# Kernel optimization log

Hardware: AMD Instinct MI355X
Metric: run time of the kernel (lower is better)

The kernel has to match this reference:

```python
import jax, jax.numpy as jnp
import numpy as np

N_NODES = 50000
N_EDGES = 800000
F = 53
B = 128
H = 4


def _p(key, shape, scale=0.1):
    return jax.random.normal(key, shape, dtype=jnp.float32) * scale


def setup_inputs() -> dict:
    key = jax.random.key(0)
    ks = jax.random.split(key, 40)
    inp = {
        'x': jax.random.normal(ks[0], (N_NODES, F), dtype=jnp.float32),
        'edge_index': jax.random.randint(ks[1], (2, N_EDGES), 0, N_NODES),
        'batch': jnp.sort(jax.random.randint(ks[2], (N_NODES,), 0, B)),
        # GATConv(53 -> 53, heads=4)
        'gat_w': _p(ks[3], (F, H * F)),
        'gat_att_src': _p(ks[4], (H, F)),
        'gat_att_dst': _p(ks[5], (H, F)),
        'gat_bias': _p(ks[6], (H * F,)),
        # GINConv MLP: 53 -> 106 -> 106
        'gin_w1': _p(ks[7], (F, 2 * F)), 'gin_b1': _p(ks[8], (2 * F,)),
        'gin_w2': _p(ks[9], (2 * F, 2 * F)), 'gin_b2': _p(ks[10], (2 * F,)),
        # EdgeConv MLP: 106 -> 106 -> 106
        'ec_w1': _p(ks[11], (2 * F, 2 * F)), 'ec_b1': _p(ks[12], (2 * F,)),
        'ec_w2': _p(ks[13], (2 * F, 2 * F)), 'ec_b2': _p(ks[14], (2 * F,)),
        # per-branch heads
        'fg1_w': _p(ks[15], (4 * F, 256)), 'fg1_b': _p(ks[16], (256,)),
        'fg2_w': _p(ks[17], (256, 128)), 'fg2_b': _p(ks[18], (128,)),
        'fg3_w': _p(ks[19], (2 * F, 256)), 'fg3_b': _p(ks[20], (256,)),
        'fg4_w': _p(ks[21], (256, 128)), 'fg4_b': _p(ks[22], (128,)),
        'fg5_w': _p(ks[23], (2 * F, 256)), 'fg5_b': _p(ks[24], (256,)),
        'fg6_w': _p(ks[25], (256, 128)), 'fg6_b': _p(ks[26], (128,)),
        # final MLP
        'fc1_w': _p(ks[27], (384, 128)), 'fc1_b': _p(ks[28], (128,)),
        'fc2_w': _p(ks[29], (128, 64)), 'fc2_b': _p(ks[30], (64,)),
        'out_w': _p(ks[31], (64, 1)), 'out_b': _p(ks[32], (1,)),
    }
    return inp


def _gat(x, src, dst, w, a_src, a_dst, bias):
    # PyG GATConv with add_self_loops=True, negative_slope=0.2, concat heads
    n = x.shape[0]
    loop = jnp.arange(n)
    s = jnp.concatenate([src, loop])
    d = jnp.concatenate([dst, loop])
    xh = (x @ w).reshape(n, H, F)                      # [N,H,F]
    al_s = jnp.einsum('nhf,hf->nh', xh, a_src)         # [N,H]
    al_d = jnp.einsum('nhf,hf->nh', xh, a_dst)
    e = jax.nn.leaky_relu(al_s[s] + al_d[d], 0.2)      # [E2,H]
    m = jax.ops.segment_max(e, d, num_segments=n)
    ex = jnp.exp(e - m[d])
    z = jax.ops.segment_sum(ex, d, num_segments=n)
    alpha = ex / (z[d] + 1e-16)                        # softmax over in-edges
    msg = xh[s] * alpha[:, :, None]                    # [E2,H,F]
    out = jax.ops.segment_sum(msg, d, num_segments=n)
    return out.reshape(n, H * F) + bias


def _gin(x, src, dst, w1, b1, w2, b2):
    # PyG GINConv, eps=0: nn(x + sum_j x_j)
    n = x.shape[0]
    agg = jax.ops.segment_sum(x[src], dst, num_segments=n)
    h = x + agg
    return jax.nn.relu(h @ w1 + b1) @ w2 + b2


def _edgeconv(x, src, dst, w1, b1, w2, b2):
    # PyG EdgeConv: max_j nn([x_i, x_j - x_i]) at target i
    n = x.shape[0]
    xi = x[dst]
    feat = jnp.concatenate([xi, x[src] - xi], axis=-1)  # [E,2F]
    h = jax.nn.relu(feat @ w1 + b1) @ w2 + b2
    out = jax.ops.segment_max(h, dst, num_segments=n)
    return jnp.where(jnp.isfinite(out), out, 0.0)       # empty segments -> 0


def _gep(x, batch):
    # global mean pool per graph
    s = jax.ops.segment_sum(x, batch, num_segments=B)
    cnt = jax.ops.segment_sum(jnp.ones((x.shape[0],), x.dtype), batch, num_segments=B)
    return s / jnp.maximum(cnt, 1.0)[:, None]


def reference(x, edge_index, batch,
              gat_w, gat_att_src, gat_att_dst, gat_bias,
              gin_w1, gin_b1, gin_w2, gin_b2,
              ec_w1, ec_b1, ec_w2, ec_b2,
              fg1_w, fg1_b, fg2_w, fg2_b, fg3_w, fg3_b,
              fg4_w, fg4_b, fg5_w, fg5_b, fg6_w, fg6_b,
              fc1_w, fc1_b, fc2_w, fc2_b, out_w, out_b):
    relu = jax.nn.relu
    src, dst = edge_index[0], edge_index[1]

    xt = relu(_gat(x, src, dst, gat_w, gat_att_src, gat_att_dst, gat_bias))
    xt = _gep(xt, batch)
    xt = relu(xt @ fg1_w + fg1_b)
    xt = relu(xt @ fg2_w + fg2_b)

    xt2 = relu(_gin(x, src, dst, gin_w1, gin_b1, gin_w2, gin_b2))
    xt2 = _gep(xt2, batch)
    xt2 = relu(xt2 @ fg3_w + fg3_b)
    xt2 = relu(xt2 @ fg4_w + fg4_b)

    xt3 = relu(_edgeconv(x, src, dst, ec_w1, ec_b1, ec_w2, ec_b2))
    xt3 = _gep(xt3, batch)
    xt3 = relu(xt3 @ fg5_w + fg5_b)
    xt3 = relu(xt3 @ fg6_w + fg6_b)

    h = jnp.concatenate([xt, xt2, xt3], axis=1)         # [B,384]
    h = relu(h @ fc1_w + fc1_b)
    h = relu(h @ fc2_w + fc2_b)
    return jax.nn.sigmoid(h @ out_w + out_b)            # [B,1]
```

## Files before the change

kernel.cpp:

```cpp
#include <hip/hip_runtime.h>
#include <hip/hip_bf16.h>
#include <math.h>

#define N_NODES 50000
#define N_EDGES 800000
#define FDIM 53
#define BATCH 128
#define HF 212
#define F2 106
#define POOLW 424
#define NPK2 220
#define PSTR 32
#define ECS 128

typedef __attribute__((ext_vector_type(8))) short short8;
typedef __attribute__((ext_vector_type(4))) float f32x4;

__device__ __forceinline__ float leaky02(float x){ return x >= 0.f ? x : 0.2f * x; }

__device__ __forceinline__ short f2bf(float x) {
  unsigned u = __float_as_uint(x);
  unsigned r = (u + 0x7fffu + ((u >> 16) & 1u)) >> 16;
  return (short)r;
}
__device__ __forceinline__ float bf2f(short b) {
  return __uint_as_float(((unsigned)(unsigned short)b) << 16);
}
__device__ __forceinline__ unsigned pk2(float a, float b) {
  union { __hip_bfloat162 h; unsigned u; } c;
  c.h = __float22bfloat162_rn(make_float2(a, b));
  return c.u;
}
__device__ __forceinline__ void ldsbar() {
  __builtin_amdgcn_s_waitcnt(0xC07F);
  __builtin_amdgcn_s_barrier();
}

__global__ void k_prep(const float* __restrict__ ec_w1, const float* __restrict__ ec_b1,
                       const float* __restrict__ gat_w, const float* __restrict__ asrc,
                       const float* __restrict__ adst,
                       float* __restrict__ Wp, float* __restrict__ bp) {
  int idx = blockIdx.x * blockDim.x + threadIdx.x;
  if (idx < FDIM * NPK2) {
    int k = idx / NPK2, j = idx % NPK2;
    float v;
    if (j < F2)            v = ec_w1[k * F2 + j] - ec_w1[(FDIM + k) * F2 + j];
    else if (j < 2 * F2)   v = ec_w1[(FDIM + k) * F2 + (j - F2)];
    else {
      int r = j - 2 * F2;
      int sd = r >> 2, h = r & 3;
      const float* av = sd ? adst : asrc;
      float acc = 0.f;
      for (int f = 0; f < FDIM; ++f)
        acc += gat_w[k * HF + h * FDIM + f] * av[h * FDIM + f];
      v = acc;
    }
    Wp[idx] = v;
  }
  if (idx < NPK2) {
    bp[idx] = (idx < F2) ? ec_b1[idx] : 0.f;
  }
}

#define GM 64
#define GN 110
#define GNP 112
#define APAD 57
__global__ __launch_bounds__(256) void k_gemm(
    const float* __restrict__ x, const float* __restrict__ Wp, const float* __restrict__ bp,
    short* __restrict__ xb, short* __restrict__ Ub, short* __restrict__ Vb,
    float* __restrict__ alS, float* __restrict__ alD) {
  __shared__ float As[GM * APAD];
  __shared__ float Ws[FDIM * GNP];
  int mb = blockIdx.x >> 1, nc = blockIdx.x & 1;
  int m0 = mb * GM, n0 = nc * GN;
  int t = threadIdx.x;
  for (int idx = t; idx < GM * FDIM; idx += 256) {
    int m = idx / FDIM, k = idx % FDIM;
    int gm = m0 + m;
    float v = (gm < N_NODES) ? x[(size_t)gm * FDIM + k] : 0.f;
    As[m * APAD + k] = v;
    if (nc == 0 && gm < N_NODES) xb[(size_t)gm * 64 + k] = f2bf(v);
  }
  for (int idx = t; idx < FDIM * GNP; idx += 256) {
    int k = idx / GNP, n = idx % GNP;
    Ws[idx] = (n < GN) ? Wp[k * NPK2 + n0 + n] : 0.f;
  }
  __syncthreads();
  int tx = t & 15, ty = t >> 4;
  int ms = tx * 4, ns = ty * 7;
  float acc[4][7];
#pragma unroll
  for (int i = 0; i < 4; i++)
#pragma unroll
    for (int j = 0; j < 7; j++) acc[i][j] = 0.f;
  for (int k = 0; k < FDIM; k++) {
    float a0 = As[(ms + 0) * APAD + k];
    float a1 = As[(ms + 1) * APAD + k];
    float a2 = As[(ms + 2) * APAD + k];
    float a3 = As[(ms + 3) * APAD + k];
    float b[7];
#pragma unroll
    for (int j = 0; j < 7; j++) b[j] = Ws[k * GNP + ns + j];
#pragma unroll
    for (int j = 0; j < 7; j++) {
      acc[0][j] += a0 * b[j];
      acc[1][j] += a1 * b[j];
      acc[2][j] += a2 * b[j];
      acc[3][j] += a3 * b[j];
    }
  }
  float bj[7];
#pragma unroll
  for (int j = 0; j < 7; j++) {
    int g = n0 + ns + j;
    bj[j] = (g < NPK2) ? bp[g] : 0.f;
  }
#pragma unroll
  for (int i = 0; i < 4; i++) {
    int gm = m0 + ms + i;
    if (gm >= N_NODES) break;
#pragma unroll
    for (int j = 0; j < 7; j++) {
      int g = n0 + ns + j;
      float v = acc[i][j] + bj[j];
      if (g < F2)             Ub[(size_t)gm * ECS + g] = f2bf(v);
      else if (g < 2 * F2)    Vb[(size_t)gm * ECS + (g - F2)] = f2bf(v);
      else if (g < 2 * F2 + 4) alS[gm * 4 + (g - 2 * F2)] = v;
      else if (g < NPK2)      alD[gm * 4 + (g - 2 * F2 - 4)] = v;
    }
  }
}

#define SCAN_BLOCKS ((N_NODES + 255) / 256)

__global__ void k_hist(const int* __restrict__ ei, int* __restrict__ histP) {
  int t = blockIdx.x * blockDim.x + threadIdx.x;
  if (t < N_EDGES) atomicAdd(&histP[ei[N_EDGES + t] << 5], 1);
}

__global__ __launch_bounds__(256) void k_scan1(const int* __restrict__ histP,
                                               const int* __restrict__ batch,
                                               int* __restrict__ rp, int* __restrict__ bsum,
                                               int* __restrict__ start) {
  __shared__ int buf[256];
  int tid = threadIdx.x;
  int idx = blockIdx.x * 256 + tid;
  int v = (idx < N_NODES) ? histP[idx << 5] : 0;
  buf[tid] = v;
  __syncthreads();
  for (int off = 1; off < 256; off <<= 1) {
    int t2 = (tid >= off) ? buf[tid - off] : 0;
    __syncthreads();
    buf[tid] += t2;
    __syncthreads();
  }
  if (idx < N_NODES) rp[idx] = buf[tid] - v;
  if (tid == 255) bsum[blockIdx.x] = buf[255];
  if (idx < N_NODES) {
    int b = batch[idx];
    if (idx == 0)
      for (int g = 0; g <= b; g++) start[g] = 0;
    int bn = (idx + 1 < N_NODES) ? batch[idx + 1] : BATCH;
    for (int g = b + 1; g <= bn; g++) start[g] = idx + 1;
  }
}

__global__ __launch_bounds__(256) void k_scan3(const int* __restrict__ bsum,
                                               int* __restrict__ rp, int* __restrict__ histP) {
  __shared__ int buf[256];
  int tid = threadIdx.x;
  int v = (tid < SCAN_BLOCKS) ? bsum[tid] : 0;
  buf[tid] = v;
  __syncthreads();
  for (int off = 1; off < 256; off <<= 1) {
    int t2 = (tid >= off) ? buf[tid - off] : 0;
    __syncthreads();
    buf[tid] += t2;
    __syncthreads();
  }
  int boff = (blockIdx.x == 0) ? 0 : buf[blockIdx.x - 1];
  int idx = blockIdx.x * 256 + tid;
  if (idx < N_NODES) {
    int o = rp[idx] + boff;
    rp[idx] = o;
    histP[idx << 5] = o;
  }
  if (idx == 0) rp[N_NODES] = N_EDGES;
}

__global__ void k_scatter(const int* __restrict__ ei, int* __restrict__ histP,
                          int* __restrict__ colidx) {
  int e = blockIdx.x * blockDim.x + threadIdx.x;
  if (e >= N_EDGES) return;
  int d = ei[N_EDGES + e];
  int pos = atomicAdd(&histP[d << 5], 1);
  colidx[pos] = ei[e];
}

#define GCH 20
__global__ __launch_bounds__(256) void k_gatgin(
    const short* __restrict__ xb, const float* __restrict__ alS, const float* __restrict__ alD,
    const int* __restrict__ rp, const int* __restrict__ colidx,
    short* __restrict__ agg4, float* __restrict__ agg) {
  int wid = threadIdx.x >> 6, lane = threadIdx.x & 63;
  bool fa = lane < FDIM;
  int i0 = blockIdx.x * GCH;
  int iend = min(i0 + GCH, N_NODES);
  __shared__ int rpG[GCH + 1];
  __shared__ int sL[4][64];
  __shared__ float4 eL[4][64];
  {
    int t = threadIdx.x, nn = iend - i0;
    if (t <= nn) rpG[t] = rp[i0 + t];
  }
  __syncthreads();
  for (int i = i0 + wid; i < iend; i += 4) {
    int base = rpG[i - i0], deg = rpG[i - i0 + 1] - base;
    float4 adv = *(const float4*)(alD + (size_t)i * 4);
    float4 asv = *(const float4*)(alS + (size_t)i * 4);
    float aldi[4] = {adv.x, adv.y, adv.z, adv.w};
    float exs[4];
    exs[0] = __expf(leaky02(asv.x + aldi[0]));
    exs[1] = __expf(leaky02(asv.y + aldi[1]));
    exs[2] = __expf(leaky02(asv.z + aldi[2]));
    exs[3] = __expf(leaky02(asv.w + aldi[3]));
    float xiv = fa ? bf2f(xb[(size_t)i * 64 + lane]) : 0.f;
    float ag0 = exs[0] * xiv, ag1 = exs[1] * xiv, ag2 = exs[2] * xiv, ag3 = exs[3] * xiv;
    float ax = xiv;
    float zl[4] = {0.f, 0.f, 0.f, 0.f};

    for (int c0 = 0; c0 < deg; c0 += 64) {
      int cn = min(64, deg - c0);
      int s = 0;
      float ex0 = 0.f, ex1 = 0.f, ex2 = 0.f, ex3 = 0.f;
      if (lane < cn) {
        s = colidx[base + c0 + lane];
        float4 av = *(const float4*)(alS + (size_t)s * 4);
        ex0 = __expf(leaky02(av.x + aldi[0]));
        ex1 = __expf(leaky02(av.y + aldi[1]));
        ex2 = __expf(leaky02(av.z + aldi[2]));
        ex3 = __expf(leaky02(av.w + aldi[3]));
        zl[0] += ex0; zl[1] += ex1; zl[2] += ex2; zl[3] += ex3;
      }
      sL[wid][lane] = s;
      eL[wid][lane] = make_float4(ex0, ex1, ex2, ex3);
      for (int jj = 0; jj < cn; jj += 4) {
        int4 s4 = *(const int4*)&sL[wid][jj];
        int sj[4] = {s4.x, s4.y, s4.z, s4.w};
        float4 e0 = eL[wid][jj + 0];
        float4 e1 = eL[wid][jj + 1];
        float4 e2 = eL[wid][jj + 2];
        float4 e3 = eL[wid][jj + 3];
        float xg[4];
#pragma unroll
        for (int q = 0; q < 4; q++)
          xg[q] = fa ? bf2f(xb[(size_t)sj[q] * 64 + lane]) : 0.f;
        ag0 += e0.x * xg[0] + e1.x * xg[1] + e2.x * xg[2] + e3.x * xg[3];
        ag1 += e0.y * xg[0] + e1.y * xg[1] + e2.y * xg[2] + e3.y * xg[3];
        ag2 += e0.z * xg[0] + e1.z * xg[1] + e2.z * xg[2] + e3.z * xg[3];
        ag3 += e0.w * xg[0] + e1.w * xg[1] + e2.w * xg[2] + e3.w * xg[3];
#pragma unroll
        for (int q = 0; q < 4; q++)
          if (jj + q < cn) ax += xg[q];
      }
    }
#pragma unroll
    for (int off = 32; off >= 1; off >>= 1)
#pragma unroll
      for (int h = 0; h < 4; h++) zl[h] += __shfl_xor(zl[h], off);
    if (fa) {
      float z0 = zl[0] + exs[0] + 1e-16f;
      float z1 = zl[1] + exs[1] + 1e-16f;
      float z2 = zl[2] + exs[2] + 1e-16f;
      float z3 = zl[3] + exs[3] + 1e-16f;
      short* ar = agg4 + (size_t)i * HF;
      ar[0 * FDIM + lane] = f2bf(ag0 / z0);
      ar[1 * FDIM + lane] = f2bf(ag1 / z1);
      ar[2 * FDIM + lane] = f2bf(ag2 / z2);
      ar[3 * FDIM + lane] = f2bf(ag3 / z3);
      agg[(size_t)i * FDIM + lane] = ax;
    }
  }
}

#define AHS 264
#define BTS 72
#define A2PAD 111
#define SMBYTES 75904
__global__ __launch_bounds__(256) void k_post(
    const short* __restrict__ agg4, const float* __restrict__ gat_w,
    const float* __restrict__ gat_b,
    const float* __restrict__ agg,
    const float* __restrict__ w1, const float* __restrict__ b1,
    const float* __restrict__ w2, const float* __restrict__ b2,
    const int* __restrict__ batch, float* __restrict__ pooled) {
  __shared__ __align__(16) char smraw[SMBYTES];
  __shared__ float psum[4 * 224];
  __shared__ int batL[64];
  int m0 = blockIdx.x * 64;
  int t = threadIdx.x;
  const int lane = t & 63, wid = t >> 6;
  const int n16 = lane & 15, quad = lane >> 4;

  {
    short* Ah = (short*)smraw;
    short* Bt = (short*)(smraw + (size_t)64 * AHS * 2);
    for (int idx = t; idx < 4 * 224; idx += 256) psum[idx] = 0.f;
    if (t < 64) batL[t] = (m0 + t < N_NODES) ? batch[m0 + t] : 0;
    for (int idx = t; idx < 64 * 256; idx += 256) {
      int node = idx >> 8, rem = idx & 255;
      int h = rem >> 6, k = rem & 63;
      int gm = m0 + node;
      short v = (k < FDIM && gm < N_NODES) ? agg4[(size_t)gm * HF + h * FDIM + k] : (short)0;
      Ah[node * AHS + h * 64 + k] = v;
    }
    for (int idx = t; idx < 4 * 56 * 64; idx += 256) {
      int h = idx / (56 * 64), rem = idx % (56 * 64);
      int n = rem >> 6, k = rem & 63;
      short v = (k < FDIM && n < FDIM) ? f2bf(gat_w[k * HF + h * FDIM + n]) : (short)0;
      Bt[(h * 56 + n) * BTS + k] = v;
    }
    __syncthreads();
    const int mrow0 = wid * 16;
    const int bmin = batL[0];
#pragma unroll
    for (int h = 0; h < 4; h++) {
      short8 af0 = *(const short8*)&Ah[(mrow0 + n16) * AHS + h * 64 + quad * 8];
      short8 af1 = *(const short8*)&Ah[(mrow0 + n16) * AHS + h * 64 + 32 + quad * 8];
#pragma unroll
      for (int nt = 0; nt < 4; nt++) {
        short8 b0 = *(const short8*)&Bt[(h * 56 + nt * 16 + n16) * BTS + quad * 8];
        short8 b1 = *(const short8*)&Bt[(h * 56 + nt * 16 + n16) * BTS + 32 + quad * 8];
        f32x4 acc = {0.f, 0.f, 0.f, 0.f};
        acc = __builtin_amdgcn_mfma_f32_16x16x32_bf16(af0, b0, acc, 0, 0, 0);
        acc = __builtin_amdgcn_mfma_f32_16x16x32_bf16(af1, b1, acc, 0, 0, 0);
        int jn = nt * 16 + n16;
        bool jv = jn < FDIM;
        float bj = jv ? gat_b[h * FDIM + jn] : 0.f;
        float pj = 0.f; int curb = -1;
#pragma unroll
        for (int r = 0; r < 4; r++) {
          int lm = mrow0 + quad * 4 + r;
          int gm = m0 + lm;
          if (gm < N_NODES) {
            float o = fmaxf(acc[r] + bj, 0.f);
            int b = batL[lm];
            if (b != curb) {
              if (curb >= 0 && jv) {
                int slot = curb - bmin;
                if (slot >= 0 && slot < 4) atomicAdd(&psum[slot * 224 + h * 56 + jn], pj);
                else atomicAdd(&pooled[(size_t)curb * POOLW + h * FDIM + jn], pj);
              }
              curb = b; pj = o;
            } else {
              pj += o;
            }
          }
        }
        if (curb >= 0 && jv) {
          int slot = curb - bmin;
          if (slot >= 0 && slot < 4) atomicAdd(&psum[slot * 224 + h * 56 + jn], pj);
          else atomicAdd(&pooled[(size_t)curb * POOLW + h * FDIM + jn], pj);
        }
      }
    }
    __syncthreads();
    for (int idx = t; idx < 4 * 224; idx += 256) {
      int slot = idx / 224, c = idx % 224;
      int h = c / 56, jn = c % 56;
      float v = psum[idx];
      int b = bmin + slot;
      if (jn < FDIM && b < BATCH && v != 0.f)
        atomicAdd(&pooled[(size_t)b * POOLW + h * FDIM + jn], v);
    }
    __syncthreads();
  }

  {
    float* B1 = (float*)smraw;
    float* Hs = (float*)(smraw + (size_t)F2 * 112 * 4);
    float* As = B1;
    float* Ws1 = B1 + 64 * APAD;
    for (int idx = t; idx < 4 * 112; idx += 256) psum[idx] = 0.f;
    for (int idx = t; idx < 64 * FDIM; idx += 256) {
      int m = idx / FDIM, k = idx % FDIM;
      int gm = m0 + m;
      As[m * APAD + k] = (gm < N_NODES) ? agg[(size_t)gm * FDIM + k] : 0.f;
    }
    for (int idx = t; idx < FDIM * 112; idx += 256) {
      int k = idx / 112, n = idx % 112;
      Ws1[idx] = (n < F2) ? w1[k * F2 + n] : 0.f;
    }
    __syncthreads();
    int tx = t & 15, ty = t >> 4;
    int ms = tx * 4, ns = ty * 7;
    {
      float acc[4][7];
#pragma unroll
      for (int i = 0; i < 4; i++)
#pragma unroll
        for (int j = 0; j < 7; j++) acc[i][j] = 0.f;
      for (int k = 0; k < FDIM; k++) {
        float a0 = As[(ms + 0) * APAD + k];
        float a1 = As[(ms + 1) * APAD + k];
        float a2 = As[(ms + 2) * APAD + k];
        float a3 = As[(ms + 3) * APAD + k];
        float b[7];
#pragma unroll
        for (int j = 0; j < 7; j++) b[j] = Ws1[k * 112 + ns + j];
#pragma unroll
        for (int j = 0; j < 7; j++) {
          acc[0][j] += a0 * b[j];
          acc[1][j] += a1 * b[j];
          acc[2][j] += a2 * b[j];
          acc[3][j] += a3 * b[j];
        }
      }
#pragma unroll
      for (int i = 0; i < 4; i++) {
#pragma unroll
        for (int j = 0; j < 7; j++) {
          int n = ns + j;
          if (n < F2) Hs[(ms + i) * A2PAD + n] = fmaxf(acc[i][j] + b1[n], 0.f);
        }
      }
    }
    __syncthreads();
    for (int idx = t; idx < F2 * 112; idx += 256) {
      int k = idx / 112, n = idx % 112;
      B1[idx] = (n < F2) ? w2[k * F2 + n] : 0.f;
    }
    __syncthreads();
    float acc[4][7];
#pragma unroll
    for (int i = 0; i < 4; i++)
#pragma unroll
      for (int j = 0; j < 7; j++) acc[i][j] = 0.f;
    for (int k = 0; k < F2; k++) {
      float a0 = Hs[(ms + 0) * A2PAD + k];
      float a1 = Hs[(ms + 1) * A2PAD + k];
      float a2 = Hs[(ms + 2) * A2PAD + k];
      float a3 = Hs[(ms + 3) * A2PAD + k];
      float b[7];
#pragma unroll
      for (int j = 0; j < 7; j++) b[j] = B1[k * 112 + ns + j];
#pragma unroll
      for (int j = 0; j < 7; j++) {
        acc[0][j] += a0 * b[j];
        acc[1][j] += a1 * b[j];
        acc[2][j] += a2 * b[j];
        acc[3][j] += a3 * b[j];
      }
    }
    float b2n[7];
#pragma unroll
    for (int j = 0; j < 7; j++) {
      int n = ns + j;
      b2n[j] = (n < F2) ? b2[n] : 0.f;
    }
    int bmin = batL[0];
    float pj[7];
#pragma unroll
    for (int j = 0; j < 7; j++) pj[j] = 0.f;
    int curb = -1;
#pragma unroll
    for (int i = 0; i < 4; i++) {
      int gm = m0 + ms + i;
      if (gm >= N_NODES) break;
      int b = batL[ms + i];
      if (b != curb) {
        if (curb >= 0) {
          int slot = curb - bmin;
          if (slot >= 0 && slot < 4) {
#pragma unroll
            for (int j = 0; j < 7; j++)
              if (ns + j < F2) atomicAdd(&psum[slot * 112 + ns + j], pj[j]);
          } else {
            float* pg = pooled + (size_t)curb * POOLW + HF;
#pragma unroll
            for (int j = 0; j < 7; j++)
              if (ns + j < F2) atomicAdd(&pg[ns + j], pj[j]);
          }
        }
        curb = b;
#pragma unroll
        for (int j = 0; j < 7; j++)
          pj[j] = (ns + j < F2) ? fmaxf(acc[i][j] + b2n[j], 0.f) : 0.f;
      } else {
#pragma unroll
        for (int j = 0; j < 7; j++)
          if (ns + j < F2) pj[j] += fmaxf(acc[i][j] + b2n[j], 0.f);
      }
    }
    if (curb >= 0) {
      int slot = curb - bmin;
      if (slot >= 0 && slot < 4) {
#pragma unroll
        for (int j = 0; j < 7; j++)
          if (ns + j < F2) atomicAdd(&psum[slot * 112 + ns + j], pj[j]);
      } else {
        float* pg = pooled + (size_t)curb * POOLW + HF;
#pragma unroll
        for (int j = 0; j < 7; j++)
          if (ns + j < F2) atomicAdd(&pg[ns + j], pj[j]);
      }
    }
    __syncthreads();
    for (int idx = t; idx < 4 * 112; idx += 256) {
      int slot = idx / 112, n = idx % 112;
      float v = psum[idx];
      int b = bmin + slot;
      if (n < F2 && b < BATCH && v != 0.f)
        atomicAdd(&pooled[(size_t)b * POOLW + HF + n], v);
    }
  }
}

#define ECH 25
__global__ __launch_bounds__(256) void k_ec(
    const short* __restrict__ Ub, const short* __restrict__ Vb,
    const float* __restrict__ w2, const float* __restrict__ b2,
    const int* __restrict__ rp, const int* __restrict__ colidx,
    const int* __restrict__ batch, float* __restrict__ pooled) {
  const int t = threadIdx.x;
  const int lane = t & 63, wid = t >> 6;
  const int n16 = lane & 15, quad = lane >> 4;
  const int nt = (wid == 3) ? 1 : 2;

  const int i0 = blockIdx.x * ECH;
  const int iend = min(i0 + ECH, N_NODES);
  const int nn = iend - i0;

  __shared__ int rpL[ECH + 1];
  __shared__ int batL[ECH];

  short8 Bh[2][4];
  for (int tt = 0; tt < 2; tt++) {
    int ucol = (wid * 2 + tt) * 16 + n16;
    for (int kc = 0; kc < 4; kc++) {
      short8 vh;
#pragma unroll
      for (int jv = 0; jv < 8; jv++) {
        int kk = kc * 32 + quad * 8 + jv;
        float w = (ucol < F2 && kk < F2) ? w2[kk * F2 + ucol] : 0.f;
        vh[jv] = f2bf(w);
      }
      Bh[tt][kc] = vh;
    }
  }
  float b2v[2];
#pragma unroll
  for (int tt = 0; tt < 2; tt++) {
    int u = (wid * 2 + tt) * 16 + n16;
    b2v[tt] = (u < F2) ? b2[u] : 0.f;
  }

  if (t <= nn) rpL[t] = rp[i0 + t];
  if (t < nn) batL[t] = batch[i0 + t];
  __syncthreads();

  __shared__ short hs[2][16 * 16 * 8];
  union SU { short8 s; unsigned u[4]; };
  const int es = t & 15, kg = t >> 4;
  const int k0 = kg * 8;

  float sm0 = 0.f, sm1 = 0.f;
  int curb = -1;
  const int u0 = (wid * 2) * 16 + n16;
  const int u1 = (wid * 2 + 1) * 16 + n16;

  auto advance = [&](int& ii, int& ttb, int& bb, int& dd) -> bool {
    ttb++;
    if (ttb * 16 < dd) return true;
    ttb = 0;
    for (ii = ii + 1; ii < iend; ii++) {
      bb = rpL[ii - i0]; dd = rpL[ii - i0 + 1] - bb;
      if (dd > 0) return true;
    }
    return false;
  };

  int i = i0, tb = 0, base = 0, deg = 0;
  bool have = false;
  for (; i < iend; i++) {
    base = rpL[i - i0]; deg = rpL[i - i0 + 1] - base;
    if (deg > 0) { have = true; break; }
  }
  short8 pu8{}, pv8{};
  int i1 = i, tb1 = 0, base1 = base, deg1 = deg;
  bool have1 = false;
  int sc = 0;
  if (have) {
    pu8 = *(const short8*)(Ub + (size_t)i * ECS + k0);
    int s0 = colidx[base + ((es < deg) ? es : 0)];
    pv8 = *(const short8*)(Vb + (size_t)s0 * ECS + k0);
    have1 = advance(i1, tb1, base1, deg1);
    if (have1) {
      int eg = tb1 * 16 + es;
      sc = colidx[base1 + ((eg < deg1) ? eg : 0)];
    }
  }

  float Uc[8];
  float vmax0 = -1e30f, vmax1 = -1e30f;
  int parity = 0;
  while (have) {
    if (tb == 0) {
#pragma unroll
      for (int j = 0; j < 8; j++) Uc[j] = bf2f(pu8[j]);
    }
    SU w;
#pragma unroll
    for (int p = 0; p < 4; p++) {
      bool kv = (k0 + 2 * p) < F2;
      float h0 = kv ? fmaxf(Uc[2 * p]     + bf2f(pv8[2 * p]),     0.f) : 0.f;
      float h1 = kv ? fmaxf(Uc[2 * p + 1] + bf2f(pv8[2 * p + 1]), 0.f) : 0.f;
      w.u[p] = pk2(h0, h1);
    }
    *(short8*)&hs[parity][(kg * 16 + es) * 8] = w.s;

    int i2 = i1, tb2 = tb1, base2 = base1, deg2 = deg1;
    bool have2 = false;
    int scN = 0;
    if (have1) {
      if (tb1 == 0) pu8 = *(const short8*)(Ub + (size_t)i1 * ECS + k0);
      pv8 = *(const short8*)(Vb + (size_t)sc * ECS + k0);
      have2 = advance(i2, tb2, base2, deg2);
      if (have2) {
        int eg2 = tb2 * 16 + es;
        scN = colidx[base2 + ((eg2 < deg2) ? eg2 : 0)];
      }
    }

    ldsbar();
    f32x4 a0 = {0.f, 0.f, 0.f, 0.f}, a1 = {0.f, 0.f, 0.f, 0.f};
#pragma unroll
    for (int kc = 0; kc < 4; kc++) {
      short8 af = *(const short8*)&hs[parity][((kc * 4 + quad) * 16 + n16) * 8];
      a0 = __builtin_amdgcn_mfma_f32_16x16x32_bf16(af, Bh[0][kc], a0, 0, 0, 0);
      if (nt > 1)
        a1 = __builtin_amdgcn_mfma_f32_16x16x32_bf16(af, Bh[1][kc], a1, 0, 0, 0);
    }
#pragma unroll
    for (int r = 0; r < 4; r++) {
      int er = tb * 16 + quad * 4 + r;
      if (er < deg) { vmax0 = fmaxf(vmax0, a0[r]); vmax1 = fmaxf(vmax1, a1[r]); }
    }
    if (!have1 || i1 != i) {
      vmax0 = fmaxf(vmax0, __shfl_xor(vmax0, 16));
      vmax0 = fmaxf(vmax0, __shfl_xor(vmax0, 32));
      vmax1 = fmaxf(vmax1, __shfl_xor(vmax1, 16));
      vmax1 = fmaxf(vmax1, __shfl_xor(vmax1, 32));
      float o0 = fmaxf(vmax0 + b2v[0], 0.f);
      float o1 = fmaxf(vmax1 + b2v[1], 0.f);
      int b = batL[i - i0];
      if (b != curb) {
        if (curb >= 0 && quad == 0) {
          float* pg = pooled + (size_t)curb * POOLW + HF + F2;
          if (u0 < F2) atomicAdd(&pg[u0], sm0);
          if (nt > 1 && u1 < F2) atomicAdd(&pg[u1], sm1);
        }
        curb = b; sm0 = o0; sm1 = o1;
      } else {
        sm0 += o0; sm1 += o1;
      }
      vmax0 = -1e30f; vmax1 = -1e30f;
    }
    i = i1; tb = tb1; base = base1; deg = deg1; have = have1;
    i1 = i2; tb1 = tb2; base1 = base2; deg1 = deg2; have1 = have2;
    sc = scN;
    parity ^= 1;
  }
  if (curb >= 0 && quad == 0) {
    float* pg = pooled + (size_t)curb * POOLW + HF + F2;
    if (u0 < F2) atomicAdd(&pg[u0], sm0);
    if (nt > 1 && u1 < F2) atomicAdd(&pg[u1], sm1);
  }
}

__global__ __launch_bounds__(256) void k_heads(
    const float* __restrict__ pooled, const int* __restrict__ start,
    const float* __restrict__ fg1_w, const float* __restrict__ fg1_b,
    const float* __restrict__ fg2_w, const float* __restrict__ fg2_b,
    const float* __restrict__ fg3_w, const float* __restrict__ fg3_b,
    const float* __restrict__ fg4_w, const float* __restrict__ fg4_b,
    const float* __restrict__ fg5_w, const float* __restrict__ fg5_b,
    const float* __restrict__ fg6_w, const float* __restrict__ fg6_b,
    const float* __restrict__ fc1_w, const float* __restrict__ fc1_b,
    const float* __restrict__ fc2_w, const float* __restrict__ fc2_b,
    const float* __restrict__ out_w, const float* __restrict__ out_b,
    float* __restrict__ out) {
  int g = blockIdx.x, t = threadIdx.x;
  __shared__ float in[POOLW];
  __shared__ float mid[256];
  __shared__ float cat[384];
  __shared__ float h1[128];
  __shared__ float h2[64];
  float c = fmaxf((float)(start[g + 1] - start[g]), 1.f);
  for (int idx = t; idx < POOLW; idx += 256)
    in[idx] = pooled[(size_t)g * POOLW + idx] / c;
  __syncthreads();
  const float* w1s[3] = {fg1_w, fg3_w, fg5_w};
  const float* b1s[3] = {fg1_b, fg3_b, fg5_b};
  const float* w2s[3] = {fg2_w, fg4_w, fg6_w};
  const float* b2s[3] = {fg2_b, fg4_b, fg6_b};
  const int off[4] = {0, HF, HF + F2, POOLW};
  for (int br = 0; br < 3; br++) {
    int kin = off[br + 1] - off[br];
    const float* iv = &in[off[br]];
    float a = b1s[br][t];
    const float* W = w1s[br];
    for (int k = 0; k < kin; k++) a += iv[k] * W[k * 256 + t];
    mid[t] = fmaxf(a, 0.f);
    __syncthreads();
    if (t < 128) {
      float b = b2s[br][t];
      const float* W2 = w2s[br];
      for (int k = 0; k < 256; k++) b += mid[k] * W2[k * 128 + t];
      cat[br * 128 + t] = fmaxf(b, 0.f);
    }
    __syncthreads();
  }
  if (t < 128) {
    float a = fc1_b[t];
    for (int k = 0; k < 384; k++) a += cat[k] * fc1_w[k * 128 + t];
    h1[t] = fmaxf(a, 0.f);
  }
  __syncthreads();
  if (t < 64) {
    float a = fc2_b[t];
    for (int k = 0; k < 128; k++) a += h1[k] * fc2_w[k * 64 + t];
    h2[t] = fmaxf(a, 0.f);
  }
  __syncthreads();
  if (t == 0) {
    float a = out_b[0];
    for (int k = 0; k < 64; k++) a += h2[k] * out_w[k];
    out[g] = 1.f / (1.f + __expf(-a));
  }
}

extern "C" void kernel_launch(void* const* d_in, const int* in_sizes, int n_in,
                              void* d_out, int out_size, void* d_ws, size_t ws_size,
                              hipStream_t stream) {
  const float* x      = (const float*)d_in[0];
  const int*   ei     = (const int*)d_in[1];
  const int*   batch  = (const int*)d_in[2];
  const float* gat_w  = (const float*)d_in[3];
  const float* asrc   = (const float*)d_in[4];
  const float* adst   = (const float*)d_in[5];
  const float* gat_b  = (const float*)d_in[6];
  const float* gin_w1 = (const float*)d_in[7];
  const float* gin_b1 = (const float*)d_in[8];
  const float* gin_w2 = (const float*)d_in[9];
  const float* gin_b2 = (const float*)d_in[10];
  const float* ec_w1  = (const float*)d_in[11];
  const float* ec_b1  = (const float*)d_in[12];
  const float* ec_w2  = (const float*)d_in[13];
  const float* ec_b2  = (const float*)d_in[14];
  const float* fg1_w = (const float*)d_in[15]; const float* fg1_b = (const float*)d_in[16];
  const float* fg2_w = (const float*)d_in[17]; const float* fg2_b = (const float*)d_in[18];
  const float* fg3_w = (const float*)d_in[19]; const float* fg3_b = (const float*)d_in[20];
  const float* fg4_w = (const float*)d_in[21]; const float* fg4_b = (const float*)d_in[22];
  const float* fg5_w = (const float*)d_in[23]; const float* fg5_b = (const float*)d_in[24];
  const float* fg6_w = (const float*)d_in[25]; const float* fg6_b = (const float*)d_in[26];
  const float* fc1_w = (const float*)d_in[27]; const float* fc1_b = (const float*)d_in[28];
  const float* fc2_w = (const float*)d_in[29]; const float* fc2_b = (const float*)d_in[30];
  const float* out_w = (const float*)d_in[31]; const float* out_b = (const float*)d_in[32];
  float* out = (float*)d_out;

  char* ws = (char*)d_ws;
  size_t off = 0;
  auto alloc = [&](size_t bytes) -> void* {
    void* p = ws + off;
    off = (off + bytes + 255) & ~(size_t)255;
    return p;
  };
  size_t zoff0 = off;
  int*   histP  = (int*)alloc((size_t)N_NODES * PSTR * sizeof(int));
  float* pooled = (float*)alloc((size_t)BATCH * POOLW * sizeof(float));
  size_t zbytes = off - zoff0;
  int*   rp     = (int*)alloc((N_NODES + 1) * sizeof(int));
  int*   start  = (int*)alloc((BATCH + 1) * sizeof(int));
  int*   bsum   = (int*)alloc(256 * sizeof(int));
  int*   colidx = (int*)alloc(N_EDGES * sizeof(int));
  short* xb     = (short*)alloc((size_t)N_NODES * 64 * sizeof(short));
  float* alS    = (float*)alloc((size_t)N_NODES * 4 * sizeof(float));
  float* alD    = (float*)alloc((size_t)N_NODES * 4 * sizeof(float));
  short* Ubuf   = (short*)alloc((size_t)N_NODES * ECS * sizeof(short));
  short* Vbuf   = (short*)alloc((size_t)N_NODES * ECS * sizeof(short));
  short* agg4   = (short*)alloc((size_t)N_NODES * HF * sizeof(short));
  float* agg    = (float*)alloc((size_t)N_NODES * FDIM * sizeof(float));
  float* Wp     = (float*)alloc((size_t)FDIM * NPK2 * sizeof(float));
  float* bpk    = (float*)alloc(NPK2 * sizeof(float));
  (void)ws_size; (void)in_sizes; (void)n_in; (void)out_size;

  hipMemsetAsync(ws + zoff0, 0, zbytes, stream);

  k_prep<<<(FDIM * NPK2 + 255) / 256, 256, 0, stream>>>(ec_w1, ec_b1, gat_w, asrc, adst,
                                                        Wp, bpk);
  k_gemm<<<((N_NODES + GM - 1) / GM) * 2, 256, 0, stream>>>(x, Wp, bpk,
                                                            xb, Ubuf, Vbuf, alS, alD);
  k_hist<<<(N_EDGES + 255) / 256, 256, 0, stream>>>(ei, histP);
  k_scan1<<<SCAN_BLOCKS, 256, 0, stream>>>(histP, batch, rp, bsum, start);
  k_scan3<<<SCAN_BLOCKS, 256, 0, stream>>>(bsum, rp, histP);
  k_scatter<<<(N_EDGES + 255) / 256, 256, 0, stream>>>(ei, histP, colidx);

  k_gatgin<<<(N_NODES + GCH - 1) / GCH, 256, 0, stream>>>(xb, alS, alD, rp, colidx,
                                                          agg4, agg);
  k_ec<<<(N_NODES + ECH - 1) / ECH, 256, 0, stream>>>(Ubuf, Vbuf, ec_w2, ec_b2, rp, colidx, batch, pooled);
  k_post<<<(N_NODES + 63) / 64, 256, 0, stream>>>(agg4, gat_w, gat_b, agg,
                                                  gin_w1, gin_b1, gin_w2, gin_b2,
                                                  batch, pooled);

  k_heads<<<BATCH, 256, 0, stream>>>(pooled, start,
                                     fg1_w, fg1_b, fg2_w, fg2_b, fg3_w, fg3_b,
                                     fg4_w, fg4_b, fg5_w, fg5_b, fg6_w, fg6_b,
                                     fc1_w, fc1_b, fc2_w, fc2_b, out_w, out_b, out);
}
```

Baseline: 701.3 us.

## Split fused post kernel into GAT and GIN kernels with padded agg4 layout

Stores the per-head GAT aggregates with a padded 64-wide stride per head, zero-filling the pad lanes, so the transform kernel can load MFMA fragments directly from global memory without staging through shared memory. The former fused post kernel is split into a GAT-transform kernel and a GIN MLP kernel, which cuts per-block shared memory and should raise occupancy. It also adds a fast path for blocks whose nodes all belong to one graph, reducing via cross-lane shuffles before the atomics. The cost is an extra kernel launch and a larger agg4 buffer.

```diff
diff --git a/kernel.cpp b/kernel.cpp
--- a/kernel.cpp
+++ b/kernel.cpp
@@ -12,6 +12,7 @@
 #define NPK2 220
 #define PSTR 32
 #define ECS 128
+#define A4P 256
 
 typedef __attribute__((ext_vector_type(8))) short short8;
 typedef __attribute__((ext_vector_type(4))) float f32x4;
@@ -269,75 +270,70 @@
     for (int off = 32; off >= 1; off >>= 1)
 #pragma unroll
       for (int h = 0; h < 4; h++) zl[h] += __shfl_xor(zl[h], off);
-    if (fa) {
+    {
       float z0 = zl[0] + exs[0] + 1e-16f;
       float z1 = zl[1] + exs[1] + 1e-16f;
       float z2 = zl[2] + exs[2] + 1e-16f;
       float z3 = zl[3] + exs[3] + 1e-16f;
-      short* ar = agg4 + (size_t)i * HF;
-      ar[0 * FDIM + lane] = f2bf(ag0 / z0);
-      ar[1 * FDIM + lane] = f2bf(ag1 / z1);
-      ar[2 * FDIM + lane] = f2bf(ag2 / z2);
-      ar[3 * FDIM + lane] = f2bf(ag3 / z3);
-      agg[(size_t)i * FDIM + lane] = ax;
-    }
-  }
-}
-
-#define AHS 264
+      short* ar = agg4 + (size_t)i * A4P;
+      ar[0 * 64 + lane] = fa ? f2bf(ag0 / z0) : (short)0;
+      ar[1 * 64 + lane] = fa ? f2bf(ag1 / z1) : (short)0;
+      ar[2 * 64 + lane] = fa ? f2bf(ag2 / z2) : (short)0;
+      ar[3 * 64 + lane] = fa ? f2bf(ag3 / z3) : (short)0;
+      if (fa) agg[(size_t)i * FDIM + lane] = ax;
+    }
+  }
+}
+
 #define BTS 72
-#define A2PAD 111
-#define SMBYTES 75904
-__global__ __launch_bounds__(256) void k_post(
+__global__ __launch_bounds__(256) void k_gt(
     const short* __restrict__ agg4, const float* __restrict__ gat_w,
-    const float* __restrict__ gat_b,
-    const float* __restrict__ agg,
-    const float* __restrict__ w1, const float* __restrict__ b1,
-    const float* __restrict__ w2, const float* __restrict__ b2,
-    const int* __restrict__ batch, float* __restrict__ pooled) {
-  __shared__ __align__(16) char smraw[SMBYTES];
+    const float* __restrict__ gat_b, const int* __restrict__ batch,
+    float* __restrict__ pooled) {
+  __shared__ short Bt[4 * 56 * BTS];
   __shared__ float psum[4 * 224];
   __shared__ int batL[64];
   int m0 = blockIdx.x * 64;
   int t = threadIdx.x;
+  for (int idx = t; idx < 4 * 224; idx += 256) psum[idx] = 0.f;
+  if (t < 64) batL[t] = batch[min(m0 + t, N_NODES - 1)];
+  for (int idx = t; idx < 4 * 64 * 56; idx += 256) {
+    int n = idx % 56, kk = (idx / 56) & 63, h = idx / (56 * 64);
+    short v = (kk < FDIM && n < FDIM) ? f2bf(gat_w[kk * HF + h * FDIM + n]) : (short)0;
+    Bt[(h * 56 + n) * BTS + kk] = v;
+  }
+  __syncthreads();
   const int lane = t & 63, wid = t >> 6;
   const int n16 = lane & 15, quad = lane >> 4;
-
-  {
-    short* Ah = (short*)smraw;
-    short* Bt = (short*)(smraw + (size_t)64 * AHS * 2);
-    for (int idx = t; idx < 4 * 224; idx += 256) psum[idx] = 0.f;
-    if (t < 64) batL[t] = (m0 + t < N_NODES) ? batch[m0 + t] : 0;
-    for (int idx = t; idx < 64 * 256; idx += 256) {
-      int node = idx >> 8, rem = idx & 255;
-      int h = rem >> 6, k = rem & 63;
-      int gm = m0 + node;
-      short v = (k < FDIM && gm < N_NODES) ? agg4[(size_t)gm * HF + h * FDIM + k] : (short)0;
-      Ah[node * AHS + h * 64 + k] = v;
-    }
-    for (int idx = t; idx < 4 * 56 * 64; idx += 256) {
-      int h = idx / (56 * 64), rem = idx % (56 * 64);
-      int n = rem >> 6, k = rem & 63;
-      short v = (k < FDIM && n < FDIM) ? f2bf(gat_w[k * HF + h * FDIM + n]) : (short)0;
-      Bt[(h * 56 + n) * BTS + k] = v;
-    }
-    __syncthreads();
-    const int mrow0 = wid * 16;
-    const int bmin = batL[0];
-#pragma unroll
-    for (int h = 0; h < 4; h++) {
-      short8 af0 = *(const short8*)&Ah[(mrow0 + n16) * AHS + h * 64 + quad * 8];
-      short8 af1 = *(const short8*)&Ah[(mrow0 + n16) * AHS + h * 64 + 32 + quad * 8];
-#pragma unroll
-      for (int nt = 0; nt < 4; nt++) {
-        short8 b0 = *(const short8*)&Bt[(h * 56 + nt * 16 + n16) * BTS + quad * 8];
-        short8 b1 = *(const short8*)&Bt[(h * 56 + nt * 16 + n16) * BTS + 32 + quad * 8];
-        f32x4 acc = {0.f, 0.f, 0.f, 0.f};
-        acc = __builtin_amdgcn_mfma_f32_16x16x32_bf16(af0, b0, acc, 0, 0, 0);
-        acc = __builtin_amdgcn_mfma_f32_16x16x32_bf16(af1, b1, acc, 0, 0, 0);
-        int jn = nt * 16 + n16;
-        bool jv = jn < FDIM;
-        float bj = jv ? gat_b[h * FDIM + jn] : 0.f;
+  const int mrow0 = wid * 16;
+  const int bmin = batL[0];
+  const bool uni = (batL[0] == batL[63]);
+  const size_t abase = (size_t)(m0 + mrow0 + n16) * A4P;
+#pragma unroll
+  for (int h = 0; h < 4; h++) {
+    short8 af0 = *(const short8*)(agg4 + abase + h * 64 + quad * 8);
+    short8 af1 = *(const short8*)(agg4 + abase + h * 64 + 32 + quad * 8);
+#pragma unroll
+    for (int nt = 0; nt < 4; nt++) {
+      short8 b0 = *(const short8*)&Bt[(h * 56 + nt * 16 + n16) * BTS + quad * 8];
+      short8 b1 = *(const short8*)&Bt[(h * 56 + nt * 16 + n16) * BTS + 32 + quad * 8];
+      f32x4 acc = {0.f, 0.f, 0.f, 0.f};
+      acc = __builtin_amdgcn_mfma_f32_16x16x32_bf16(af0, b0, acc, 0, 0, 0);
+      acc = __builtin_amdgcn_mfma_f32_16x16x32_bf16(af1, b1, acc, 0, 0, 0);
+      int jn = nt * 16 + n16;
+      bool jv = jn < FDIM;
+      float bj = jv ? gat_b[h * FDIM + jn] : 0.f;
+      if (uni) {
+        float s = 0.f;
+#pragma unroll
+        for (int r = 0; r < 4; r++) {
+          int gm = m0 + mrow0 + quad * 4 + r;
+          if (gm < N_NODES) s += fmaxf(acc[r] + bj, 0.f);
+        }
+        s += __shfl_xor(s, 16);
+        s += __shfl_xor(s, 32);
+        if (quad == 0 && jv && s != 0.f) atomicAdd(&psum[h * 56 + jn], s);
+      } else {
         float pj = 0.f; int curb = -1;
 #pragma unroll
         for (int r = 0; r < 4; r++) {
@@ -365,86 +361,58 @@
         }
       }
     }
-    __syncthreads();
-    for (int idx = t; idx < 4 * 224; idx += 256) {
-      int slot = idx / 224, c = idx % 224;
-      int h = c / 56, jn = c % 56;
-      float v = psum[idx];
-      int b = bmin + slot;
-      if (jn < FDIM && b < BATCH && v != 0.f)
-        atomicAdd(&pooled[(size_t)b * POOLW + h * FDIM + jn], v);
-    }
-    __syncthreads();
-  }
-
+  }
+  __syncthreads();
+  for (int idx = t; idx < 4 * 224; idx += 256) {
+    int slot = idx / 224, c = idx % 224;
+    int h = c / 56, jn = c % 56;
+    float v = psum[idx];
+    int b = bmin + slot;
+    if (jn < FDIM && b < BATCH && v != 0.f)
+      atomicAdd(&pooled[(size_t)b * POOLW + h * FDIM + jn], v);
+  }
+}
+
+#define A2PAD 111
+__global__ __launch_bounds__(256) void k_gin(
+    const float* __restrict__ agg,
+    const float* __restrict__ w1, const float* __restrict__ b1,
+    const float* __restrict__ w2, const float* __restrict__ b2,
+    const int* __restrict__ batch, float* __restrict__ pooled) {
+  __shared__ float B1[F2 * 112];
+  __shared__ float Hs[64 * A2PAD];
+  __shared__ float psum[4 * 112];
+  float* As = B1;
+  float* Ws1 = B1 + 64 * APAD;
+  int m0 = blockIdx.x * 64;
+  int t = threadIdx.x;
+  for (int idx = t; idx < 4 * 112; idx += 256) psum[idx] = 0.f;
+  for (int idx = t; idx < 64 * FDIM; idx += 256) {
+    int m = idx / FDIM, k = idx % FDIM;
+    int gm = m0 + m;
+    As[m * APAD + k] = (gm < N_NODES) ? agg[(size_t)gm * FDIM + k] : 0.f;
+  }
+  for (int idx = t; idx < FDIM * 112; idx += 256) {
+    int k = idx / 112, n = idx % 112;
+    Ws1[idx] = (n < F2) ? w1[k * F2 + n] : 0.f;
+  }
+  __syncthreads();
+  int tx = t & 15, ty = t >> 4;
+  int ms = tx * 4, ns = ty * 7;
   {
-    float* B1 = (float*)smraw;
-    float* Hs = (float*)(smraw + (size_t)F2 * 112 * 4);
-    float* As = B1;
-    float* Ws1 = B1 + 64 * APAD;
-    for (int idx = t; idx < 4 * 112; idx += 256) psum[idx] = 0.f;
-    for (int idx = t; idx < 64 * FDIM; idx += 256) {
-      int m = idx / FDIM, k = idx % FDIM;
-      int gm = m0 + m;
-      As[m * APAD + k] = (gm < N_NODES) ? agg[(size_t)gm * FDIM + k] : 0.f;
-    }
-    for (int idx = t; idx < FDIM * 112; idx += 256) {
-      int k = idx / 112, n = idx % 112;
-      Ws1[idx] = (n < F2) ? w1[k * F2 + n] : 0.f;
-    }
-    __syncthreads();
-    int tx = t & 15, ty = t >> 4;
-    int ms = tx * 4, ns = ty * 7;
-    {
-      float acc[4][7];
-#pragma unroll
-      for (int i = 0; i < 4; i++)
-#pragma unroll
-        for (int j = 0; j < 7; j++) acc[i][j] = 0.f;
-      for (int k = 0; k < FDIM; k++) {
-        float a0 = As[(ms + 0) * APAD + k];
-        float a1 = As[(ms + 1) * APAD + k];
-        float a2 = As[(ms + 2) * APAD + k];
-        float a3 = As[(ms + 3) * APAD + k];
-        float b[7];
-#pragma unroll
-        for (int j = 0; j < 7; j++) b[j] = Ws1[k * 112 + ns + j];
-#pragma unroll
-        for (int j = 0; j < 7; j++) {
-          acc[0][j] += a0 * b[j];
-          acc[1][j] += a1 * b[j];
-          acc[2][j] += a2 * b[j];
-          acc[3][j] += a3 * b[j];
-        }
-      }
-#pragma unroll
-      for (int i = 0; i < 4; i++) {
-#pragma unroll
-        for (int j = 0; j < 7; j++) {
-          int n = ns + j;
-          if (n < F2) Hs[(ms + i) * A2PAD + n] = fmaxf(acc[i][j] + b1[n], 0.f);
-        }
-      }
-    }
-    __syncthreads();
-    for (int idx = t; idx < F2 * 112; idx += 256) {
-      int k = idx / 112, n = idx % 112;
-      B1[idx] = (n < F2) ? w2[k * F2 + n] : 0.f;
-    }
-    __syncthreads();
     float acc[4][7];
 #pragma unroll
     for (int i = 0; i < 4; i++)
 #pragma unroll
       for (int j = 0; j < 7; j++) acc[i][j] = 0.f;
-    for (int k = 0; k < F2; k++) {
-      float a0 = Hs[(ms + 0) * A2PAD + k];
-      float a1 = Hs[(ms + 1) * A2PAD + k];
-      float a2 = Hs[(ms + 2) * A2PAD + k];
-      float a3 = Hs[(ms + 3) * A2PAD + k];
+    for (int k = 0; k < FDIM; k++) {
+      float a0 = As[(ms + 0) * APAD + k];
+      float a1 = As[(ms + 1) * APAD + k];
+      float a2 = As[(ms + 2) * APAD + k];
+      float a3 = As[(ms + 3) * APAD + k];
       float b[7];
 #pragma unroll
-      for (int j = 0; j < 7; j++) b[j] = B1[k * 112 + ns + j];
+      for (int j = 0; j < 7; j++) b[j] = Ws1[k * 112 + ns + j];
 #pragma unroll
       for (int j = 0; j < 7; j++) {
         acc[0][j] += a0 * b[j];
@@ -453,67 +421,102 @@
         acc[3][j] += a3 * b[j];
       }
     }
-    float b2n[7];
+#pragma unroll
+    for (int i = 0; i < 4; i++) {
+#pragma unroll
+      for (int j = 0; j < 7; j++) {
+        int n = ns + j;
+        if (n < F2) Hs[(ms + i) * A2PAD + n] = fmaxf(acc[i][j] + b1[n], 0.f);
+      }
+    }
+  }
+  __syncthreads();
+  for (int idx = t; idx < F2 * 112; idx += 256) {
+    int k = idx / 112, n = idx % 112;
+    B1[idx] = (n < F2) ? w2[k * F2 + n] : 0.f;
+  }
+  __syncthreads();
+  float acc[4][7];
+#pragma unroll
+  for (int i = 0; i < 4; i++)
+#pragma unroll
+    for (int j = 0; j < 7; j++) acc[i][j] = 0.f;
+  for (int k = 0; k < F2; k++) {
+    float a0 = Hs[(ms + 0) * A2PAD + k];
+    float a1 = Hs[(ms + 1) * A2PAD + k];
+    float a2 = Hs[(ms + 2) * A2PAD + k];
+    float a3 = Hs[(ms + 3) * A2PAD + k];
+    float b[7];
+#pragma unroll
+    for (int j = 0; j < 7; j++) b[j] = B1[k * 112 + ns + j];
 #pragma unroll
     for (int j = 0; j < 7; j++) {
-      int n = ns + j;
-      b2n[j] = (n < F2) ? b2[n] : 0.f;
-    }
-    int bmin = batL[0];
-    float pj[7];
-#pragma unroll
-    for (int j = 0; j < 7; j++) pj[j] = 0.f;
-    int curb = -1;
-#pragma unroll
-    for (int i = 0; i < 4; i++) {
-      int gm = m0 + ms + i;
-      if (gm >= N_NODES) break;
-      int b = batL[ms + i];
-      if (b != curb) {
-        if (curb >= 0) {
-          int slot = curb - bmin;
-          if (slot >= 0 && slot < 4) {
-#pragma unroll
-            for (int j = 0; j < 7; j++)
-              if (ns + j < F2) atomicAdd(&psum[slot * 112 + ns + j], pj[j]);
-          } else {
-            float* pg = pooled + (size_t)curb * POOLW + HF;
-#pragma unroll
-            for (int j = 0; j < 7; j++)
-              if (ns + j < F2) atomicAdd(&pg[ns + j], pj[j]);
-          }
+      acc[0][j] += a0 * b[j];
+      acc[1][j] += a1 * b[j];
+      acc[2][j] += a2 * b[j];
+      acc[3][j] += a3 * b[j];
+    }
+  }
+  float b2n[7];
+#pragma unroll
+  for (int j = 0; j < 7; j++) {
+    int n = ns + j;
+    b2n[j] = (n < F2) ? b2[n] : 0.f;
+  }
+  int bmin = batch[m0];
+  float pj[7];
+#pragma unroll
+  for (int j = 0; j < 7; j++) pj[j] = 0.f;
+  int curb = -1;
+#pragma unroll
+  for (int i = 0; i < 4; i++) {
+    int gm = m0 + ms + i;
+    if (gm >= N_NODES) break;
+    int b = batch[gm];
+    if (b != curb) {
+      if (curb >= 0) {
+        int slot = curb - bmin;
+        if (slot >= 0 && slot < 4) {
+#pragma unroll
+          for (int j = 0; j < 7; j++)
+            if (ns + j < F2) atomicAdd(&psum[slot * 112 + ns + j], pj[j]);
+        } else {
+          float* pg = pooled + (size_t)curb * POOLW + HF;
+#pragma unroll
+          for (int j = 0; j < 7; j++)
+            if (ns + j < F2) atomicAdd(&pg[ns + j], pj[j]);
         }
-        curb = b;
-#pragma unroll
-        for (int j = 0; j < 7; j++)
-          pj[j] = (ns + j < F2) ? fmaxf(acc[i][j] + b2n[j], 0.f) : 0.f;
-      } else {
-#pragma unroll
-        for (int j = 0; j < 7; j++)
-          if (ns + j < F2) pj[j] += fmaxf(acc[i][j] + b2n[j], 0.f);
       }
-    }
-    if (curb >= 0) {
-      int slot = curb - bmin;
-      if (slot >= 0 && slot < 4) {
-#pragma unroll
-        for (int j = 0; j < 7; j++)
-          if (ns + j < F2) atomicAdd(&psum[slot * 112 + ns + j], pj[j]);
-      } else {
-        float* pg = pooled + (size_t)curb * POOLW + HF;
-#pragma unroll
-        for (int j = 0; j < 7; j++)
-          if (ns + j < F2) atomicAdd(&pg[ns + j], pj[j]);
-      }
-    }
-    __syncthreads();
-    for (int idx = t; idx < 4 * 112; idx += 256) {
-      int slot = idx / 112, n = idx % 112;
-      float v = psum[idx];
-      int b = bmin + slot;
-      if (n < F2 && b < BATCH && v != 0.f)
-        atomicAdd(&pooled[(size_t)b * POOLW + HF + n], v);
-    }
+      curb = b;
+#pragma unroll
+      for (int j = 0; j < 7; j++)
+        pj[j] = (ns + j < F2) ? fmaxf(acc[i][j] + b2n[j], 0.f) : 0.f;
+    } else {
+#pragma unroll
+      for (int j = 0; j < 7; j++)
+        if (ns + j < F2) pj[j] += fmaxf(acc[i][j] + b2n[j], 0.f);
+    }
+  }
+  if (curb >= 0) {
+    int slot = curb - bmin;
+    if (slot >= 0 && slot < 4) {
+#pragma unroll
+      for (int j = 0; j < 7; j++)
+        if (ns + j < F2) atomicAdd(&psum[slot * 112 + ns + j], pj[j]);
+    } else {
+      float* pg = pooled + (size_t)curb * POOLW + HF;
+#pragma unroll
+      for (int j = 0; j < 7; j++)
+        if (ns + j < F2) atomicAdd(&pg[ns + j], pj[j]);
+    }
+  }
+  __syncthreads();
+  for (int idx = t; idx < 4 * 112; idx += 256) {
+    int slot = idx / 112, n = idx % 112;
+    float v = psum[idx];
+    int b = bmin + slot;
+    if (n < F2 && b < BATCH && v != 0.f)
+      atomicAdd(&pooled[(size_t)b * POOLW + HF + n], v);
   }
 }
 
@@ -790,7 +793,7 @@
   float* alD    = (float*)alloc((size_t)N_NODES * 4 * sizeof(float));
   short* Ubuf   = (short*)alloc((size_t)N_NODES * ECS * sizeof(short));
   short* Vbuf   = (short*)alloc((size_t)N_NODES * ECS * sizeof(short));
-  short* agg4   = (short*)alloc((size_t)N_NODES * HF * sizeof(short));
+  short* agg4   = (short*)alloc((size_t)(N_NODES + 64) * A4P * sizeof(short));
   float* agg    = (float*)alloc((size_t)N_NODES * FDIM * sizeof(float));
   float* Wp     = (float*)alloc((size_t)FDIM * NPK2 * sizeof(float));
   float* bpk    = (float*)alloc(NPK2 * sizeof(float));
@@ -810,9 +813,9 @@
   k_gatgin<<<(N_NODES + GCH - 1) / GCH, 256, 0, stream>>>(xb, alS, alD, rp, colidx,
                                                           agg4, agg);
   k_ec<<<(N_NODES + ECH - 1) / ECH, 256, 0, stream>>>(Ubuf, Vbuf, ec_w2, ec_b2, rp, colidx, batch, pooled);
-  k_post<<<(N_NODES + 63) / 64, 256, 0, stream>>>(agg4, gat_w, gat_b, agg,
-                                                  gin_w1, gin_b1, gin_w2, gin_b2,
-                                                  batch, pooled);
+  k_gt<<<(N_NODES + 63) / 64, 256, 0, stream>>>(agg4, gat_w, gat_b, batch, pooled);
+  k_gin<<<(N_NODES + 63) / 64, 256, 0, stream>>>(agg, gin_w1, gin_b1, gin_w2, gin_b2,
+                                                 batch, pooled);
 
   k_heads<<<BATCH, 256, 0, stream>>>(pooled, start,
                                      fg1_w, fg1_b, fg2_w, fg2_b, fg3_w, fg3_b,
```

New measurement: 649.0 us. -7.5%, faster.
